# Performance work log

Measured on AMD Instinct MI355X. Metric: run time of the kernel, lower is better.

## Reference

```python
import jax, jax.numpy as jnp
from jax import lax
import numpy as np

B, CIN, COUT, D, TDIM, E = 2, 16, 8, 96, 256, 8


def setup_inputs() -> dict:
    key = jax.random.key(0)
    ks = jax.random.split(key, 12)
    s = lambda fan: 1.0 / np.sqrt(fan)
    return {
        "x": jax.random.normal(ks[0], (B, CIN, D, D, D), jnp.float32),
        "text_features": jax.random.normal(ks[1], (B, TDIM), jnp.float32),
        # expert weight basis [E, Cout, Cin, 3, 3, 3] (kaiming-uniform-ish)
        "weight_basis": jax.random.uniform(ks[2], (E, COUT, CIN, 3, 3, 3), jnp.float32, -s(CIN * 27), s(CIN * 27)),
        "bias_basis": jnp.zeros((E, COUT), jnp.float32),
        # router MLP: text_dim -> 64 -> E
        "r_w1": jax.random.uniform(ks[3], (TDIM, 64), jnp.float32, -s(TDIM), s(TDIM)),
        "r_b1": jax.random.uniform(ks[4], (64,), jnp.float32, -s(TDIM), s(TDIM)),
        "r_w2": jax.random.uniform(ks[5], (64, E), jnp.float32, -s(64), s(64)),
        "r_b2": jax.random.uniform(ks[6], (E,), jnp.float32, -s(64), s(64)),
        # modulator MLP: text_dim -> 64 -> Cout
        "m_w1": jax.random.uniform(ks[7], (TDIM, 64), jnp.float32, -s(TDIM), s(TDIM)),
        "m_b1": jax.random.uniform(ks[8], (64,), jnp.float32, -s(TDIM), s(TDIM)),
        "m_w2": jax.random.uniform(ks[9], (64, COUT), jnp.float32, -s(64), s(64)),
        "m_b2": jax.random.uniform(ks[10], (COUT,), jnp.float32, -s(64), s(64)),
    }


def reference(x, text_features, weight_basis, bias_basis,
              r_w1, r_b1, r_w2, r_b2, m_w1, m_b1, m_w2, m_b2):
    b, cin = x.shape[0], x.shape[1]
    cout = weight_basis.shape[1]
    # router -> softmax routing weights over experts
    h = jax.nn.leaky_relu(text_features @ r_w1 + r_b1, 0.1)
    router_logits = h @ r_w2 + r_b2                      # [b, E]
    routing_weights = jax.nn.softmax(router_logits, -1)  # [b, E]
    # modulator -> per-sample channel gates
    g = jax.nn.leaky_relu(text_features @ m_w1 + m_b1, 0.1)
    gamma = jax.nn.sigmoid(g @ m_w2 + m_b2)              # [b, Cout]
    # per-sample dynamic conv weights via expert mixing
    cw = jnp.einsum('be,eoixyz->boixyz', routing_weights, weight_basis)  # [b,Cout,Cin,3,3,3]
    cb = routing_weights @ bias_basis                                    # [b, Cout]
    # grouped-conv trick: batch folded into channels, groups=b
    xr = x.reshape(1, b * cin, *x.shape[2:])
    wr = cw.reshape(b * cout, cin, 3, 3, 3)
    out = lax.conv_general_dilated(
        xr, wr, window_strides=(1, 1, 1), padding=[(1, 1)] * 3,
        dimension_numbers=('NCDHW', 'OIDHW', 'NCDHW'), feature_group_count=b)
    out = out.reshape(b, cout, *out.shape[2:]) + cb[:, :, None, None, None]
    out = out * (1.0 + gamma[:, :, None, None, None])
    return out, router_logits, routing_weights
```

## Files before the change

kernel.cpp:

```cpp
#include <hip/hip_runtime.h>
#include <math.h>

#define NB 2
#define CIN 16
#define COUT 8
#define DD 96
#define TDIM 256
#define NE 8
#define VOX (DD*DD*DD)
#define OUT_ELEMS (NB*COUT*VOX)

#define WS_A_F 7168
#define WS_D_F 7184

#define LX 18
#define PLANE (LX*LX)
#define NVX (PLANE*5)
#define HALFB (NVX*16)

#define MWN (COUT*CIN*27)

typedef _Float16 f16x8 __attribute__((ext_vector_type(8)));
typedef _Float16 f16x4 __attribute__((ext_vector_type(4)));
typedef float f32x4 __attribute__((ext_vector_type(4)));

__global__ __launch_bounds__(256) void setup_kernel(
    const float* __restrict__ text,
    const float* __restrict__ wb,
    const float* __restrict__ bb,
    const float* __restrict__ rw1, const float* __restrict__ rb1,
    const float* __restrict__ rw2, const float* __restrict__ rb2,
    const float* __restrict__ mw1, const float* __restrict__ mb1,
    const float* __restrict__ mw2, const float* __restrict__ mb2,
    float* __restrict__ dout_tail,
    char* __restrict__ tab)
{
    __shared__ struct {
        float mw[MWN];
        float part[256];
        float hg[2][64];
        float logits[NE];
        float rwv[NE];
    } s;
    const int t = threadIdx.x;
    const int b = blockIdx.x;

    {
        const int o = t & 127;
        const int which = o >> 6, j = o & 63;
        const int kh = t >> 7;
        const float* __restrict__ w1 = which ? mw1 : rw1;
        const float* __restrict__ tx = text + b*TDIM + kh*128;
        const float* __restrict__ wp = w1 + (size_t)(kh*128)*64 + j;
        float a0 = 0.f, a1 = 0.f, a2 = 0.f, a3 = 0.f;
        #pragma unroll 8
        for (int k = 0; k < 128; k += 4) {
            a0 = fmaf(tx[k+0], wp[(k+0)*64], a0);
            a1 = fmaf(tx[k+1], wp[(k+1)*64], a1);
            a2 = fmaf(tx[k+2], wp[(k+2)*64], a2);
            a3 = fmaf(tx[k+3], wp[(k+3)*64], a3);
        }
        s.part[t] = (a0 + a1) + (a2 + a3);
    }
    __syncthreads();
    if (t < 128) {
        const int which = t >> 6, j = t & 63;
        float acc = (which ? mb1 : rb1)[j] + s.part[t] + s.part[t + 128];
        s.hg[which][j] = (acc >= 0.f) ? acc : 0.1f * acc;
    }
    __syncthreads();
    if (t < NE) {
        float acc = rb2[t];
        #pragma unroll
        for (int k = 0; k < 64; ++k) acc = fmaf(s.hg[0][k], rw2[k*NE + t], acc);
        s.logits[t] = acc;
        dout_tail[b*NE + t] = acc;
    }
    __syncthreads();
    if (t < NE) {
        float mx = s.logits[0];
        for (int k = 1; k < NE; ++k) mx = fmaxf(mx, s.logits[k]);
        float ssum = 0.f;
        for (int k = 0; k < NE; ++k) ssum += expf(s.logits[k] - mx);
        const float w = expf(s.logits[t] - mx) / ssum;
        s.rwv[t] = w;
        dout_tail[NB*NE + b*NE + t] = w;
    }
    __syncthreads();
    float rv[NE];
    #pragma unroll
    for (int e = 0; e < NE; ++e) rv[e] = s.rwv[e];

    if (t < COUT) {
        float acc = mb2[t];
        #pragma unroll
        for (int k = 0; k < 64; ++k) acc = fmaf(s.hg[1][k], mw2[k*COUT + t], acc);
        const float gamma = 1.f / (1.f + expf(-acc));
        const float a = 1.f + gamma;
        float cb = 0.f;
        #pragma unroll
        for (int e = 0; e < NE; ++e) cb = fmaf(rv[e], bb[e*COUT + t], cb);
        ((float*)tab)[WS_A_F + b*COUT + t] = a;
        ((float*)tab)[WS_D_F + b*COUT + t] = cb * a;
    }

    #pragma unroll
    for (int i0 = 0; i0 < (MWN + 255)/256; ++i0) {
        const int i = i0*256 + t;
        if (i < MWN) {
            float v = 0.f;
            #pragma unroll
            for (int e = 0; e < NE; ++e) v = fmaf(rv[e], wb[e*MWN + i], v);
            s.mw[i] = v;
        }
    }
    __syncthreads();

    for (int r = t; r < 14*64*8; r += 256) {
        const int c  = r >> 9;
        const int l  = (r >> 3) & 63;
        const int j  = r & 7;
        const int q  = l >> 4;
        const int n  = l & 15;
        const int p  = q & 1;
        const int ci = (q >> 1)*8 + j;
        int tap;
        if (c < 9)        tap = (c/3)*9 + (c%3)*3 + p;
        else if (c < 12)  tap = (c-9)*9 + p*3 + 2;
        else if (c == 12) tap = p*9 + 8;
        else              tap = p ? -1 : 26;
        float v = 0.f;
        if (n < 8 && tap >= 0) v = s.mw[(n*CIN + ci)*27 + tap];
        ((_Float16*)tab)[b*7168 + r] = (_Float16)v;
    }
}

__global__ __launch_bounds__(256) void conv_mfma(
    const float* __restrict__ x,
    const char* __restrict__ tab,
    float* __restrict__ out)
{
    __shared__ char lds[2*HALFB];
    const int tid  = threadIdx.x;
    const int lane = tid & 63;
    const int wv   = tid >> 6;
    const int b    = blockIdx.z;
    const int z0   = blockIdx.y * 3;
    const int xti  = blockIdx.x % 6;
    const int yti  = blockIdx.x / 6;
    const int x0   = xti * 16, y0 = yti * 16;

    const f16x8* __restrict__ bfp = (const f16x8*)tab;
    f16x8 bfrag[14];
    #pragma unroll
    for (int c = 0; c < 14; ++c)
        bfrag[c] = bfp[(b*14 + c)*64 + lane];

    const float* __restrict__ xb = x + (size_t)b * CIN * VOX;
    for (int sv = tid; sv < NVX; sv += 256) {
        const int lz = sv / PLANE;
        const int r1 = sv - lz * PLANE;
        const int ly = r1 / LX;
        const int lx = r1 - ly * LX;
        const int zg = z0 - 1 + lz, yg = y0 - 1 + ly, xg = x0 - 1 + lx;
        const bool ok = ((unsigned)zg < 96u) & ((unsigned)yg < 96u) & ((unsigned)xg < 96u);
        union { _Float16 h[16]; uint4 uu[2]; } o;
        o.uu[0] = make_uint4(0u,0u,0u,0u);
        o.uu[1] = make_uint4(0u,0u,0u,0u);
        if (ok) {
            const float* __restrict__ gp = xb + (size_t)((zg*DD + yg)*DD + xg);
            #pragma unroll
            for (int ci = 0; ci < CIN; ++ci)
                o.h[ci] = (_Float16)gp[(size_t)ci * VOX];
        }
        *(uint4*)&lds[sv*16]         = o.uu[0];
        *(uint4*)&lds[HALFB + sv*16] = o.uu[1];
    }
    __syncthreads();

    const int q    = lane >> 4;
    const int m    = lane & 15;
    const int pbit = q & 1;
    const int hbit = q >> 1;

    const float* tabf = (const float*)tab;
    const float a_n = tabf[WS_A_F + b*8 + (m & 7)];
    const float d_n = tabf[WS_D_F + b*8 + (m & 7)];

    const int com = hbit*HALFB + m*16;
    const int dA = pbit*16;
    const int dB = pbit*288;
    const int dC = pbit*5184;

    #define LD_A(p_, dy_)  (*(const f16x8*)&lds[((p_)*PLANE + (yi+(dy_))*LX)*16 + com + dA])
    #define LD_G(p_)       (*(const f16x8*)&lds[((p_)*PLANE + yi*LX + 2)*16 + com + dB])
    #define LD_H12(zi_)    (*(const f16x8*)&lds[((zi_)*PLANE + (yi+2)*LX + 2)*16 + com + dC])
    #define LD_H13(zi_)    (*(const f16x8*)&lds[(((zi_)+2)*PLANE + (yi+2)*LX + 2)*16 + com])

    #pragma unroll
    for (int yi4 = 0; yi4 < 4; ++yi4) {
        const int yi = wv*4 + yi4;

        f16x8 A[3][3], G[3];
        #pragma unroll
        for (int dy = 0; dy < 3; ++dy) { A[0][dy] = LD_A(0, dy); A[1][dy] = LD_A(1, dy); }
        G[0] = LD_G(0); G[1] = LD_G(1);

        #pragma unroll
        for (int zi = 0; zi < 3; ++zi) {
            #pragma unroll
            for (int dy = 0; dy < 3; ++dy) A[2][dy] = LD_A(zi+2, dy);
            G[2] = LD_G(zi+2);
            const f16x8 H12v = LD_H12(zi);
            const f16x8 H13v = LD_H13(zi);

            f32x4 acc0 = {0.f,0.f,0.f,0.f}, acc1 = {0.f,0.f,0.f,0.f};
            acc0 = __builtin_amdgcn_mfma_f32_16x16x32_f16(A[0][0], bfrag[0],  acc0, 0,0,0);
            acc1 = __builtin_amdgcn_mfma_f32_16x16x32_f16(A[0][1], bfrag[1],  acc1, 0,0,0);
            acc0 = __builtin_amdgcn_mfma_f32_16x16x32_f16(A[0][2], bfrag[2],  acc0, 0,0,0);
            acc1 = __builtin_amdgcn_mfma_f32_16x16x32_f16(A[1][0], bfrag[3],  acc1, 0,0,0);
            acc0 = __builtin_amdgcn_mfma_f32_16x16x32_f16(A[1][1], bfrag[4],  acc0, 0,0,0);
            acc1 = __builtin_amdgcn_mfma_f32_16x16x32_f16(A[1][2], bfrag[5],  acc1, 0,0,0);
            acc0 = __builtin_amdgcn_mfma_f32_16x16x32_f16(A[2][0], bfrag[6],  acc0, 0,0,0);
            acc1 = __builtin_amdgcn_mfma_f32_16x16x32_f16(A[2][1], bfrag[7],  acc1, 0,0,0);
            acc0 = __builtin_amdgcn_mfma_f32_16x16x32_f16(A[2][2], bfrag[8],  acc0, 0,0,0);
            acc1 = __builtin_amdgcn_mfma_f32_16x16x32_f16(G[0],    bfrag[9],  acc1, 0,0,0);
            acc0 = __builtin_amdgcn_mfma_f32_16x16x32_f16(G[1],    bfrag[10], acc0, 0,0,0);
            acc1 = __builtin_amdgcn_mfma_f32_16x16x32_f16(G[2],    bfrag[11], acc1, 0,0,0);
            acc0 = __builtin_amdgcn_mfma_f32_16x16x32_f16(H12v,    bfrag[12], acc0, 0,0,0);
            acc1 = __builtin_amdgcn_mfma_f32_16x16x32_f16(H13v,    bfrag[13], acc1, 0,0,0);

            if (m < 8) {
                const int zz = z0 + zi, yy = y0 + yi;
                float* __restrict__ op = out + (size_t)(b*COUT + m)*VOX
                                            + (size_t)(zz*DD + yy)*DD + x0 + q*4;
                f32x4 res;
                #pragma unroll
                for (int r = 0; r < 4; ++r) res[r] = fmaf(acc0[r] + acc1[r], a_n, d_n);
                *reinterpret_cast<f32x4*>(op) = res;
            }

            #pragma unroll
            for (int dy = 0; dy < 3; ++dy) { A[0][dy] = A[1][dy]; A[1][dy] = A[2][dy]; }
            G[0] = G[1]; G[1] = G[2];
        }
    }
    #undef LD_A
    #undef LD_G
    #undef LD_H12
    #undef LD_H13
}

extern "C" void kernel_launch(void* const* d_in, const int* in_sizes, int n_in,
                              void* d_out, int out_size, void* d_ws, size_t ws_size,
                              hipStream_t stream) {
    const float* x    = (const float*)d_in[0];
    const float* text = (const float*)d_in[1];
    const float* wb   = (const float*)d_in[2];
    const float* bb   = (const float*)d_in[3];
    const float* rw1  = (const float*)d_in[4];
    const float* rb1  = (const float*)d_in[5];
    const float* rw2  = (const float*)d_in[6];
    const float* rb2  = (const float*)d_in[7];
    const float* mw1  = (const float*)d_in[8];
    const float* mb1  = (const float*)d_in[9];
    const float* mw2  = (const float*)d_in[10];
    const float* mb2  = (const float*)d_in[11];

    float* out = (float*)d_out;
    char* tab = (char*)d_ws;

    setup_kernel<<<dim3(NB), 256, 0, stream>>>(
        text, wb, bb, rw1, rb1, rw2, rb2, mw1, mb1, mw2, mb2,
        out + OUT_ELEMS, tab);

    conv_mfma<<<dim3(36, 32, NB), 256, 0, stream>>>(x, tab, out);
}
```

Measured before the change: 269.6 us.

## Pre-transpose input to channel-last fp16 in setup kernel before conv

The setup kernel now also converts x from NCDHW fp32 into a channel-last fp16 buffer in workspace, with each voxel holding 16 channels in 32 bytes. Extra blocks do this work while one block per batch still computes the router and mixed weights. The conv kernel's halo load then reads two contiguous 16-byte vectors per voxel instead of 16 strided scalar fp32 loads. This adds a full extra pass over x (read fp32, write fp16) plus a workspace buffer, in exchange for coalesced and cheaper halo loads that are repeated across overlapping tiles.

```diff
diff --git a/kernel.cpp b/kernel.cpp
--- a/kernel.cpp
+++ b/kernel.cpp
@@ -10,6 +10,7 @@
 #define VOX (DD*DD*DD)
 #define OUT_ELEMS (NB*COUT*VOX)
 
+#define XT_BYTES ((size_t)NB * VOX * 32)
 #define WS_A_F 7168
 #define WS_D_F 7184
 
@@ -18,13 +19,16 @@
 #define NVX (PLANE*5)
 #define HALFB (NVX*16)
 
+#define NTB3 (VOX/512)
+
 #define MWN (COUT*CIN*27)
 
 typedef _Float16 f16x8 __attribute__((ext_vector_type(8)));
 typedef _Float16 f16x4 __attribute__((ext_vector_type(4)));
 typedef float f32x4 __attribute__((ext_vector_type(4)));
 
-__global__ __launch_bounds__(256) void setup_kernel(
+__global__ __launch_bounds__(256) void transpose_setup(
+    const float* __restrict__ x, _Float16* __restrict__ xt,
     const float* __restrict__ text,
     const float* __restrict__ wb,
     const float* __restrict__ bb,
@@ -43,100 +47,124 @@
         float rwv[NE];
     } s;
     const int t = threadIdx.x;
-    const int b = blockIdx.x;
-
-    {
-        const int o = t & 127;
-        const int which = o >> 6, j = o & 63;
-        const int kh = t >> 7;
-        const float* __restrict__ w1 = which ? mw1 : rw1;
-        const float* __restrict__ tx = text + b*TDIM + kh*128;
-        const float* __restrict__ wp = w1 + (size_t)(kh*128)*64 + j;
-        float a0 = 0.f, a1 = 0.f, a2 = 0.f, a3 = 0.f;
-        #pragma unroll 8
-        for (int k = 0; k < 128; k += 4) {
-            a0 = fmaf(tx[k+0], wp[(k+0)*64], a0);
-            a1 = fmaf(tx[k+1], wp[(k+1)*64], a1);
-            a2 = fmaf(tx[k+2], wp[(k+2)*64], a2);
-            a3 = fmaf(tx[k+3], wp[(k+3)*64], a3);
-        }
-        s.part[t] = (a0 + a1) + (a2 + a3);
+    const int b = blockIdx.y;
+
+    if (blockIdx.x == NTB3) {
+        {
+            const int o = t & 127;
+            const int which = o >> 6, j = o & 63;
+            const int kh = t >> 7;
+            const float* __restrict__ w1 = which ? mw1 : rw1;
+            const float* __restrict__ tx = text + b*TDIM + kh*128;
+            const float* __restrict__ wp = w1 + (size_t)(kh*128)*64 + j;
+            float a0 = 0.f, a1 = 0.f, a2 = 0.f, a3 = 0.f;
+            #pragma unroll 8
+            for (int k = 0; k < 128; k += 4) {
+                a0 = fmaf(tx[k+0], wp[(k+0)*64], a0);
+                a1 = fmaf(tx[k+1], wp[(k+1)*64], a1);
+                a2 = fmaf(tx[k+2], wp[(k+2)*64], a2);
+                a3 = fmaf(tx[k+3], wp[(k+3)*64], a3);
+            }
+            s.part[t] = (a0 + a1) + (a2 + a3);
+        }
+        __syncthreads();
+        if (t < 128) {
+            const int which = t >> 6, j = t & 63;
+            float acc = (which ? mb1 : rb1)[j] + s.part[t] + s.part[t + 128];
+            s.hg[which][j] = (acc >= 0.f) ? acc : 0.1f * acc;
+        }
+        __syncthreads();
+        if (t < NE) {
+            float acc = rb2[t];
+            #pragma unroll
+            for (int k = 0; k < 64; ++k) acc = fmaf(s.hg[0][k], rw2[k*NE + t], acc);
+            s.logits[t] = acc;
+            dout_tail[b*NE + t] = acc;
+        }
+        __syncthreads();
+        if (t < NE) {
+            float mx = s.logits[0];
+            for (int k = 1; k < NE; ++k) mx = fmaxf(mx, s.logits[k]);
+            float ssum = 0.f;
+            for (int k = 0; k < NE; ++k) ssum += expf(s.logits[k] - mx);
+            const float w = expf(s.logits[t] - mx) / ssum;
+            s.rwv[t] = w;
+            dout_tail[NB*NE + b*NE + t] = w;
+        }
+        __syncthreads();
+        float rv[NE];
+        #pragma unroll
+        for (int e = 0; e < NE; ++e) rv[e] = s.rwv[e];
+
+        if (t < COUT) {
+            float acc = mb2[t];
+            #pragma unroll
+            for (int k = 0; k < 64; ++k) acc = fmaf(s.hg[1][k], mw2[k*COUT + t], acc);
+            const float gamma = 1.f / (1.f + expf(-acc));
+            const float a = 1.f + gamma;
+            float cb = 0.f;
+            #pragma unroll
+            for (int e = 0; e < NE; ++e) cb = fmaf(rv[e], bb[e*COUT + t], cb);
+            ((float*)tab)[WS_A_F + b*COUT + t] = a;
+            ((float*)tab)[WS_D_F + b*COUT + t] = cb * a;
+        }
+
+        #pragma unroll
+        for (int i0 = 0; i0 < (MWN + 255)/256; ++i0) {
+            const int i = i0*256 + t;
+            if (i < MWN) {
+                float v = 0.f;
+                #pragma unroll
+                for (int e = 0; e < NE; ++e) v = fmaf(rv[e], wb[e*MWN + i], v);
+                s.mw[i] = v;
+            }
+        }
+        __syncthreads();
+
+        for (int r = t; r < 14*64*8; r += 256) {
+            const int c  = r >> 9;
+            const int l  = (r >> 3) & 63;
+            const int j  = r & 7;
+            const int q  = l >> 4;
+            const int n  = l & 15;
+            const int p  = q & 1;
+            const int ci = (q >> 1)*8 + j;
+            int tap;
+            if (c < 9)        tap = (c/3)*9 + (c%3)*3 + p;
+            else if (c < 12)  tap = (c-9)*9 + p*3 + 2;
+            else if (c == 12) tap = p*9 + 8;
+            else              tap = p ? -1 : 26;
+            float v = 0.f;
+            if (n < 8 && tap >= 0) v = s.mw[(n*CIN + ci)*27 + tap];
+            ((_Float16*)tab)[b*7168 + r] = (_Float16)v;
+        }
+        return;
     }
-    __syncthreads();
-    if (t < 128) {
-        const int which = t >> 6, j = t & 63;
-        float acc = (which ? mb1 : rb1)[j] + s.part[t] + s.part[t + 128];
-        s.hg[which][j] = (acc >= 0.f) ? acc : 0.1f * acc;
+
+    const int vh = blockIdx.x * 256 + t;
+    const float* __restrict__ xb = x + (size_t)b * CIN * VOX;
+
+    float2 f[CIN];
+    #pragma unroll
+    for (int ci = 0; ci < CIN; ++ci)
+        f[ci] = ((const float2*)(xb + (size_t)ci * VOX))[vh];
+
+    union { _Float16 h[16]; uint4 u[2]; } o0, o1;
+    #pragma unroll
+    for (int ci = 0; ci < CIN; ++ci) {
+        o0.h[ci] = (_Float16)f[ci].x;
+        o1.h[ci] = (_Float16)f[ci].y;
     }
-    __syncthreads();
-    if (t < NE) {
-        float acc = rb2[t];
-        #pragma unroll
-        for (int k = 0; k < 64; ++k) acc = fmaf(s.hg[0][k], rw2[k*NE + t], acc);
-        s.logits[t] = acc;
-        dout_tail[b*NE + t] = acc;
-    }
-    __syncthreads();
-    if (t < NE) {
-        float mx = s.logits[0];
-        for (int k = 1; k < NE; ++k) mx = fmaxf(mx, s.logits[k]);
-        float ssum = 0.f;
-        for (int k = 0; k < NE; ++k) ssum += expf(s.logits[k] - mx);
-        const float w = expf(s.logits[t] - mx) / ssum;
-        s.rwv[t] = w;
-        dout_tail[NB*NE + b*NE + t] = w;
-    }
-    __syncthreads();
-    float rv[NE];
-    #pragma unroll
-    for (int e = 0; e < NE; ++e) rv[e] = s.rwv[e];
-
-    if (t < COUT) {
-        float acc = mb2[t];
-        #pragma unroll
-        for (int k = 0; k < 64; ++k) acc = fmaf(s.hg[1][k], mw2[k*COUT + t], acc);
-        const float gamma = 1.f / (1.f + expf(-acc));
-        const float a = 1.f + gamma;
-        float cb = 0.f;
-        #pragma unroll
-        for (int e = 0; e < NE; ++e) cb = fmaf(rv[e], bb[e*COUT + t], cb);
-        ((float*)tab)[WS_A_F + b*COUT + t] = a;
-        ((float*)tab)[WS_D_F + b*COUT + t] = cb * a;
-    }
-
-    #pragma unroll
-    for (int i0 = 0; i0 < (MWN + 255)/256; ++i0) {
-        const int i = i0*256 + t;
-        if (i < MWN) {
-            float v = 0.f;
-            #pragma unroll
-            for (int e = 0; e < NE; ++e) v = fmaf(rv[e], wb[e*MWN + i], v);
-            s.mw[i] = v;
-        }
-    }
-    __syncthreads();
-
-    for (int r = t; r < 14*64*8; r += 256) {
-        const int c  = r >> 9;
-        const int l  = (r >> 3) & 63;
-        const int j  = r & 7;
-        const int q  = l >> 4;
-        const int n  = l & 15;
-        const int p  = q & 1;
-        const int ci = (q >> 1)*8 + j;
-        int tap;
-        if (c < 9)        tap = (c/3)*9 + (c%3)*3 + p;
-        else if (c < 12)  tap = (c-9)*9 + p*3 + 2;
-        else if (c == 12) tap = p*9 + 8;
-        else              tap = p ? -1 : 26;
-        float v = 0.f;
-        if (n < 8 && tap >= 0) v = s.mw[(n*CIN + ci)*27 + tap];
-        ((_Float16*)tab)[b*7168 + r] = (_Float16)v;
-    }
+
+    uint4* __restrict__ dst = (uint4*)(xt + (size_t)b * VOX * 16) + (size_t)vh * 4;
+    dst[0] = o0.u[0];
+    dst[1] = o0.u[1];
+    dst[2] = o1.u[0];
+    dst[3] = o1.u[1];
 }
 
 __global__ __launch_bounds__(256) void conv_mfma(
-    const float* __restrict__ x,
+    const _Float16* __restrict__ xt,
     const char* __restrict__ tab,
     float* __restrict__ out)
 {
@@ -156,7 +184,7 @@
     for (int c = 0; c < 14; ++c)
         bfrag[c] = bfp[(b*14 + c)*64 + lane];
 
-    const float* __restrict__ xb = x + (size_t)b * CIN * VOX;
+    const _Float16* __restrict__ xtb = xt + (size_t)b * VOX * 16;
     for (int sv = tid; sv < NVX; sv += 256) {
         const int lz = sv / PLANE;
         const int r1 = sv - lz * PLANE;
@@ -164,17 +192,12 @@
         const int lx = r1 - ly * LX;
         const int zg = z0 - 1 + lz, yg = y0 - 1 + ly, xg = x0 - 1 + lx;
         const bool ok = ((unsigned)zg < 96u) & ((unsigned)yg < 96u) & ((unsigned)xg < 96u);
-        union { _Float16 h[16]; uint4 uu[2]; } o;
-        o.uu[0] = make_uint4(0u,0u,0u,0u);
-        o.uu[1] = make_uint4(0u,0u,0u,0u);
-        if (ok) {
-            const float* __restrict__ gp = xb + (size_t)((zg*DD + yg)*DD + xg);
-            #pragma unroll
-            for (int ci = 0; ci < CIN; ++ci)
-                o.h[ci] = (_Float16)gp[(size_t)ci * VOX];
-        }
-        *(uint4*)&lds[sv*16]         = o.uu[0];
-        *(uint4*)&lds[HALFB + sv*16] = o.uu[1];
+        const int zc = ok ? zg : 0, yc = ok ? yg : 0, xc = ok ? xg : 0;
+        const uint4* __restrict__ p = (const uint4*)(xtb + (size_t)((zc*DD + yc)*DD + xc) * 16);
+        uint4 lo = {0,0,0,0}, hi = {0,0,0,0};
+        if (ok) { lo = p[0]; hi = p[1]; }
+        *(uint4*)&lds[sv*16]         = lo;
+        *(uint4*)&lds[HALFB + sv*16] = hi;
     }
     __syncthreads();
 
@@ -268,11 +291,12 @@
     const float* mb2  = (const float*)d_in[11];
 
     float* out = (float*)d_out;
-    char* tab = (char*)d_ws;
-
-    setup_kernel<<<dim3(NB), 256, 0, stream>>>(
-        text, wb, bb, rw1, rb1, rw2, rb2, mw1, mb1, mw2, mb2,
+    _Float16* xt = (_Float16*)d_ws;
+    char* tab = (char*)d_ws + XT_BYTES;
+
+    transpose_setup<<<dim3(NTB3 + 1, NB), 256, 0, stream>>>(
+        x, xt, text, wb, bb, rw1, rb1, rw2, rb2, mw1, mb1, mw2, mb2,
         out + OUT_ELEMS, tab);
 
-    conv_mfma<<<dim3(36, 32, NB), 256, 0, stream>>>(x, tab, out);
+    conv_mfma<<<dim3(36, 32, NB), 256, 0, stream>>>(xt, tab, out);
 }
```

Measured after the change: 249.7 us. 1.08x faster.
